# Kernel tuning notes

Hardware: AMD Instinct MI355X
Metric: run time of the kernel (lower is better)

The kernel has to match this reference:

```python
import jax, jax.numpy as jnp
import numpy as np

E, H, L, B = 2048, 32, 1024, 4
S = E // H  # 64
DM, DD = 32, 64


def _ln(x, w, b, eps=1e-5):
    m = x.mean(-1, keepdims=True)
    v = ((x - m) ** 2).mean(-1, keepdims=True)
    return (x - m) / jnp.sqrt(v + eps) * w + b


def setup_inputs() -> dict:
    key = jax.random.key(0)
    ks = jax.random.split(key, 24)
    sc = 0.02  # weight scale for stability
    d = {
        'x': jax.random.normal(ks[0], (B, L, E), jnp.float32),
        'state': jax.random.normal(ks[1], (B, 2 + S, E), jnp.float32) * 0.1,
        'ln1_w': jnp.ones((E,), jnp.float32), 'ln1_b': jnp.zeros((E,), jnp.float32),
        'ln2_w': jnp.ones((E,), jnp.float32), 'ln2_b': jnp.zeros((E,), jnp.float32),
        'maa_x': jax.random.normal(ks[2], (E,), jnp.float32) * 0.1,
        'maa_w1': jax.random.normal(ks[3], (E, 5 * DM), jnp.float32) * sc,
        'maa_w2': jax.random.normal(ks[4], (5, DM, E), jnp.float32) * sc,
        'maa_stack': jax.random.normal(ks[5], (1, 5, E), jnp.float32) * 0.1,
        'time_decay': jax.random.normal(ks[6], (E,), jnp.float32) * 0.5,
        'td_w1': jax.random.normal(ks[7], (E, DD), jnp.float32) * sc,
        'td_w2': jax.random.normal(ks[8], (DD, E), jnp.float32) * sc,
        'u': jax.random.normal(ks[9], (H, S, 1), jnp.float32) * 0.1,
        'Wr': jax.random.normal(ks[10], (E, E), jnp.float32) * sc,
        'Wk': jax.random.normal(ks[11], (E, E), jnp.float32) * sc,
        'Wv': jax.random.normal(ks[12], (E, E), jnp.float32) * sc,
        'Wg': jax.random.normal(ks[13], (E, E), jnp.float32) * sc,
        'Wo': jax.random.normal(ks[14], (E, E), jnp.float32) * sc,
        'gn_w': jnp.ones((E,), jnp.float32), 'gn_b': jnp.zeros((E,), jnp.float32),
        'ffn_maa_k': jax.random.normal(ks[15], (E,), jnp.float32) * 0.1,
        'ffn_maa_r': jax.random.normal(ks[16], (E,), jnp.float32) * 0.1,
        'Wfk': jax.random.normal(ks[17], (E, E), jnp.float32) * sc,
        'Wfr': jax.random.normal(ks[18], (E, E), jnp.float32) * sc,
        'Wfv': jax.random.normal(ks[19], (E, E), jnp.float32) * sc,
    }
    return d


def _block(x, state, ln1_w, ln1_b, ln2_w, ln2_b, maa_x, maa_w1, maa_w2, maa_stack,
           time_decay, td_w1, td_w2, u, Wr, Wk, Wv, Wg, Wo, gn_w, gn_b,
           ffn_maa_k, ffn_maa_r, Wfk, Wfr, Wfv):
    b, l, e = x.shape
    h = u.shape[0]
    s_ = e // h
    # ---- time mixing (parallel over L, sequential WKV scan) ----
    xa = _ln(x, ln1_w, ln1_b)
    # token shift: sx[t] = x[t-1] - x[t], seeded from state row 1
    sx = jnp.concatenate([state[:, 1:2] - xa[:, :1], xa[:, :-1] - xa[:, 1:]], axis=1)
    xxx = jnp.tanh((xa + sx * maa_x) @ maa_w1).reshape(b, l, 5, DM)
    xxx = jnp.einsum('blfd,fde->blfe', xxx, maa_w2)            # [B,L,5,E]
    xm = xa[:, :, None] + sx[:, :, None] * (maa_stack + xxx)   # [B,L,5,E]
    xk, xw, xv, xr, xg = (xm[:, :, j] for j in range(5))       # stack order: k,w,v,r,g
    w = jnp.exp(-jnp.exp(time_decay + jnp.tanh(xw @ td_w1) @ td_w2)).reshape(b, l, h, s_)
    r = (xr @ Wr.T).reshape(b, l, h, s_)
    k = (xk @ Wk.T).reshape(b, l, h, s_)
    v = (xv @ Wv.T).reshape(b, l, h, s_)
    g = jax.nn.silu(xg @ Wg.T)                                 # [B,L,E]
    s0 = state[:, 2:2 + s_].reshape(b, h, s_, s_)              # per-head WKV state

    def step(s, rkvw):
        r_t, k_t, v_t, w_t = rkvw                              # each [B,H,S]
        a = k_t[..., :, None] * v_t[..., None, :]              # outer product [B,H,S,S]
        out = jnp.einsum('bhi,bhij->bhj', r_t, u * a + s)      # [B,H,S]
        s = a + w_t[..., :, None] * s
        return s, out

    rkvw = tuple(jnp.moveaxis(t, 1, 0) for t in (r, k, v, w))  # [L,B,H,S]
    _, out = jax.lax.scan(step, s0, rkvw)
    out = jnp.moveaxis(out, 0, 1).reshape(b, l, e)             # [B,L,E]
    # group norm over heads (eps=1e-5)
    og = out.reshape(b, l, h, s_)
    m = og.mean(-1, keepdims=True)
    va = ((og - m) ** 2).mean(-1, keepdims=True)
    og = ((og - m) / jnp.sqrt(va + 1e-5)).reshape(b, l, e) * gn_w + gn_b
    x1 = x + (og * g) @ Wo.T
    # ---- channel mixing ----
    xc = _ln(x1, ln2_w, ln2_b)
    sx2 = jnp.concatenate([state[:, 0:1] - xc[:, :1], xc[:, :-1] - xc[:, 1:]], axis=1)
    xk2 = xc + sx2 * ffn_maa_k
    xr2 = xc + sx2 * ffn_maa_r
    rr = jax.nn.sigmoid(xr2 @ Wfr.T)
    kk = jnp.square(jax.nn.relu(xk2 @ Wfk.T))
    return x1 + rr * (kk @ Wfv.T)


def reference(x, state, ln1_w, ln1_b, ln2_w, ln2_b, maa_x, maa_w1, maa_w2, maa_stack,
              time_decay, td_w1, td_w2, u, Wr, Wk, Wv, Wg, Wo, gn_w, gn_b,
              ffn_maa_k, ffn_maa_r, Wfk, Wfr, Wfv):
    return _block(x, state, ln1_w, ln1_b, ln2_w, ln2_b, maa_x, maa_w1, maa_w2, maa_stack,
                  time_decay, td_w1, td_w2, u, Wr, Wk, Wv, Wg, Wo, gn_w, gn_b,
                  ffn_maa_k, ffn_maa_r, Wfk, Wfr, Wfv)
```

## Files before the change

### kernel.cpp

```cpp
#include <hip/hip_runtime.h>


#define E     2048
#define LL    1024
#define HHH   32
#define SSS   64
#define NBL   4096
#define NBLE  8388608

typedef short bf16x8 __attribute__((ext_vector_type(8)));
typedef float f32x4  __attribute__((ext_vector_type(4)));
using u16 = unsigned short;

__device__ __forceinline__ u16 f2b(float f) {
    union { float f; unsigned int u; } c; c.f = f;
    unsigned int u = c.u;
    unsigned int r = (u + 0x7fffu + ((u >> 16) & 1u)) >> 16;
    return (u16)r;
}
__device__ __forceinline__ float b2f(u16 b) {
    union { unsigned int u; float f; } c; c.u = ((unsigned int)b) << 16; return c.f;
}

__device__ __forceinline__ float wave_sum(float v) {
#pragma unroll
    for (int m = 32; m >= 1; m >>= 1) v += __shfl_xor(v, m, 64);
    return v;
}

__device__ __forceinline__ void gl_lds16(const void* g, void* l) {
    __builtin_amdgcn_global_load_lds((const __attribute__((address_space(1))) unsigned int*)g,
                                     (__attribute__((address_space(3))) unsigned int*)l, 16, 0, 0);
}


__global__ __launch_bounds__(256) void k_convert(const float* __restrict__ in,
                                                 u16* __restrict__ out, int n) {
    int i = (blockIdx.x * 256 + threadIdx.x) * 4;
    if (i >= n) return;
    float4 v = *reinterpret_cast<const float4*>(in + i);
    ushort4 o = make_ushort4(f2b(v.x), f2b(v.y), f2b(v.z), f2b(v.w));
    *reinterpret_cast<ushort4*>(out + i) = o;
}

__global__ __launch_bounds__(256) void k_transpose(const float* __restrict__ in,
                                                   u16* __restrict__ out, int R, int C) {
    int i = blockIdx.x * 256 + threadIdx.x;
    if (i >= R * C) return;
    int r = i / C, c = i - r * C;
    out[c * R + r] = f2b(in[i]);
}

__global__ __launch_bounds__(256) void k_ln(const float* __restrict__ x,
                                            const float* __restrict__ w,
                                            const float* __restrict__ b,
                                            float* __restrict__ out) {
    int row = blockIdx.x, tid = threadIdx.x;
    const float* xr = x + (size_t)row * E + tid * 8;
    float4 v0 = *reinterpret_cast<const float4*>(xr);
    float4 v1 = *reinterpret_cast<const float4*>(xr + 4);
    float s = v0.x + v0.y + v0.z + v0.w + v1.x + v1.y + v1.z + v1.w;
    __shared__ float red[4];
    s = wave_sum(s);
    int wid = tid >> 6, lane = tid & 63;
    if (lane == 0) red[wid] = s;
    __syncthreads();
    float mean = (red[0] + red[1] + red[2] + red[3]) * (1.0f / E);
    __syncthreads();
    float q = 0.f;
    q += (v0.x - mean) * (v0.x - mean); q += (v0.y - mean) * (v0.y - mean);
    q += (v0.z - mean) * (v0.z - mean); q += (v0.w - mean) * (v0.w - mean);
    q += (v1.x - mean) * (v1.x - mean); q += (v1.y - mean) * (v1.y - mean);
    q += (v1.z - mean) * (v1.z - mean); q += (v1.w - mean) * (v1.w - mean);
    q = wave_sum(q);
    if (lane == 0) red[wid] = q;
    __syncthreads();
    float inv = rsqrtf((red[0] + red[1] + red[2] + red[3]) * (1.0f / E) + 1e-5f);
    int e = tid * 8;
    float4 w0 = *reinterpret_cast<const float4*>(w + e);
    float4 w1 = *reinterpret_cast<const float4*>(w + e + 4);
    float4 b0 = *reinterpret_cast<const float4*>(b + e);
    float4 b1 = *reinterpret_cast<const float4*>(b + e + 4);
    float4 o0, o1;
    o0.x = (v0.x - mean) * inv * w0.x + b0.x; o0.y = (v0.y - mean) * inv * w0.y + b0.y;
    o0.z = (v0.z - mean) * inv * w0.z + b0.z; o0.w = (v0.w - mean) * inv * w0.w + b0.w;
    o1.x = (v1.x - mean) * inv * w1.x + b1.x; o1.y = (v1.y - mean) * inv * w1.y + b1.y;
    o1.z = (v1.z - mean) * inv * w1.z + b1.z; o1.w = (v1.w - mean) * inv * w1.w + b1.w;
    float* op = out + (size_t)row * E + e;
    *reinterpret_cast<float4*>(op) = o0;
    *reinterpret_cast<float4*>(op + 4) = o1;
}

__global__ __launch_bounds__(256) void k_mk(const float* __restrict__ xa,
                                            const float* __restrict__ state,
                                            const float* __restrict__ maa_x,
                                            u16* __restrict__ out) {
    int i = (blockIdx.x * 256 + threadIdx.x) * 4;
    if (i >= NBLE) return;
    int n = i >> 11, e = i & (E - 1);
    int l = n & (LL - 1), b = n >> 10;
    float4 cur = *reinterpret_cast<const float4*>(xa + i);
    float4 prev;
    if (l > 0) prev = *reinterpret_cast<const float4*>(xa + i - E);
    else       prev = *reinterpret_cast<const float4*>(state + (size_t)b * 66 * E + E + e);
    float4 m = *reinterpret_cast<const float4*>(maa_x + e);
    ushort4 o = make_ushort4(f2b(cur.x + (prev.x - cur.x) * m.x),
                             f2b(cur.y + (prev.y - cur.y) * m.y),
                             f2b(cur.z + (prev.z - cur.z) * m.z),
                             f2b(cur.w + (prev.w - cur.w) * m.w));
    *reinterpret_cast<ushort4*>(out + i) = o;
}

__global__ __launch_bounds__(256) void k_mix2(const float* __restrict__ xc,
                                              const float* __restrict__ state,
                                              const float* __restrict__ mk,
                                              const float* __restrict__ mr,
                                              u16* __restrict__ xk2,
                                              u16* __restrict__ xr2) {
    int i = (blockIdx.x * 256 + threadIdx.x) * 4;
    if (i >= NBLE) return;
    int n = i >> 11, e = i & (E - 1);
    int l = n & (LL - 1), b = n >> 10;
    float4 cur = *reinterpret_cast<const float4*>(xc + i);
    float4 prev;
    if (l > 0) prev = *reinterpret_cast<const float4*>(xc + i - E);
    else       prev = *reinterpret_cast<const float4*>(state + (size_t)b * 66 * E + e);
    float4 sx = make_float4(prev.x - cur.x, prev.y - cur.y, prev.z - cur.z, prev.w - cur.w);
    float4 k4 = *reinterpret_cast<const float4*>(mk + e);
    float4 r4 = *reinterpret_cast<const float4*>(mr + e);
    ushort4 ok = make_ushort4(f2b(cur.x + sx.x * k4.x), f2b(cur.y + sx.y * k4.y),
                              f2b(cur.z + sx.z * k4.z), f2b(cur.w + sx.w * k4.w));
    ushort4 orr = make_ushort4(f2b(cur.x + sx.x * r4.x), f2b(cur.y + sx.y * r4.y),
                               f2b(cur.z + sx.z * r4.z), f2b(cur.w + sx.w * r4.w));
    *reinterpret_cast<ushort4*>(xk2 + i) = ok;
    *reinterpret_cast<ushort4*>(xr2 + i) = orr;
}

__global__ __launch_bounds__(256) void k_gnorm(const float* __restrict__ wkv,
                                               const u16* __restrict__ g,
                                               const float* __restrict__ gw,
                                               const float* __restrict__ gb,
                                               u16* __restrict__ ogg) {
    int gidx = blockIdx.x * 4 + (threadIdx.x >> 6);
    int lane = threadIdx.x & 63;
    int n = gidx >> 5, h = gidx & 31;
    size_t base = (size_t)n * E + h * SSS;
    float v = wkv[base + lane];
    float mean = wave_sum(v) * (1.0f / SSS);
    float d = v - mean;
    float var = wave_sum(d * d) * (1.0f / SSS);
    float norm = d * rsqrtf(var + 1e-5f);
    int e = h * SSS + lane;
    float res = norm * gw[e] + gb[e];
    float gv = b2f(g[base + lane]);
    ogg[base + lane] = f2b(res * gv);
}

#define CT 16

__global__ __launch_bounds__(512) void k_scan(const u16* __restrict__ Rb,
                                              const u16* __restrict__ Kb,
                                              const u16* __restrict__ Vb,
                                              const float* __restrict__ W,
                                              const float* __restrict__ state,
                                              const float* __restrict__ u,
                                              float* __restrict__ out) {
    __shared__ u16   ldsR[2][CT * 64];
    __shared__ u16   ldsK[2][CT * 64];
    __shared__ float ldsW[2][CT * 64];
    __shared__ u16   ldsV[2][CT * 32];
    const int blk = blockIdx.x;
    const int b = blk >> 6;
    const int rem = blk & 63;
    const int h = rem >> 1, jh = rem & 1;
    const int tid = threadIdx.x;
    const int wvid = tid >> 6;
    const int lane = tid & 63;
    const int ig = lane >> 2;
    const int jl = lane & 3;
    const int jv = wvid * 4 + jl;
    const int j  = jh * 32 + jv;
    const int i0 = ig * 4;
    float s[4], uu[4];
    const float* s0 = state + (size_t)b * 66 * E + 2 * E + h * (SSS * SSS);
#pragma unroll
    for (int ii = 0; ii < 4; ii++) {
        s[ii] = s0[(i0 + ii) * SSS + j];
        uu[ii] = u[h * SSS + i0 + ii];
    }
    const size_t off0 = (size_t)b * LL * E + h * SSS;

    auto stage = [&](int c, int bufsel) {
        size_t base = off0 + (size_t)c * CT * E;
        if (wvid == 0) {
            const u16* g0 = Rb + base + (size_t)(lane >> 3) * E + ((lane & 7) << 3);
            gl_lds16(g0,         &ldsR[bufsel][lane * 8]);
            gl_lds16(g0 + 8 * E, &ldsR[bufsel][512 + lane * 8]);
        } else if (wvid == 1) {
            const u16* g0 = Kb + base + (size_t)(lane >> 3) * E + ((lane & 7) << 3);
            gl_lds16(g0,         &ldsK[bufsel][lane * 8]);
            gl_lds16(g0 + 8 * E, &ldsK[bufsel][512 + lane * 8]);
        } else if (wvid == 2) {
            const float* g0 = W + base + (size_t)(lane >> 4) * E + ((lane & 15) << 2);
            gl_lds16(g0,         &ldsW[bufsel][lane * 4]);
            gl_lds16(g0 + 4 * E, &ldsW[bufsel][256 + lane * 4]);
        } else if (wvid == 3) {
            const float* g0 = W + base + (size_t)(8 + (lane >> 4)) * E + ((lane & 15) << 2);
            gl_lds16(g0,         &ldsW[bufsel][512 + lane * 4]);
            gl_lds16(g0 + 4 * E, &ldsW[bufsel][768 + lane * 4]);
        } else if (wvid == 4) {
            const u16* g0 = Vb + base + (size_t)(lane >> 2) * E + jh * 32 + ((lane & 3) << 3);
            gl_lds16(g0, &ldsV[bufsel][lane * 8]);
        }
    };

    stage(0, 0);
    __syncthreads();
    int cur = 0;
    for (int c = 0; c < LL / CT; c++) {
        if (c + 1 < LL / CT) stage(c + 1, cur ^ 1);
        size_t offt = off0 + (size_t)c * CT * E + j;
#pragma unroll
        for (int tt = 0; tt < CT; tt++) {
            ushort4 rv = *reinterpret_cast<const ushort4*>(&ldsR[cur][tt * 64 + i0]);
            ushort4 kv = *reinterpret_cast<const ushort4*>(&ldsK[cur][tt * 64 + i0]);
            float4  wv = *reinterpret_cast<const float4*>(&ldsW[cur][tt * 64 + i0]);
            float vj = b2f(ldsV[cur][tt * 32 + jv]);
            float acc = 0.f, a;
            a = b2f(kv.x) * vj; acc += b2f(rv.x) * fmaf(uu[0], a, s[0]); s[0] = fmaf(wv.x, s[0], a);
            a = b2f(kv.y) * vj; acc += b2f(rv.y) * fmaf(uu[1], a, s[1]); s[1] = fmaf(wv.y, s[1], a);
            a = b2f(kv.z) * vj; acc += b2f(rv.z) * fmaf(uu[2], a, s[2]); s[2] = fmaf(wv.z, s[2], a);
            a = b2f(kv.w) * vj; acc += b2f(rv.w) * fmaf(uu[3], a, s[3]); s[3] = fmaf(wv.w, s[3], a);
            acc += __shfl_xor(acc, 4, 64);
            acc += __shfl_xor(acc, 8, 64);
            acc += __shfl_xor(acc, 16, 64);
            acc += __shfl_xor(acc, 32, 64);
            if (ig == 0) out[offt + (size_t)tt * E] = acc;
        }
        __syncthreads();
        cur ^= 1;
    }
}

template <int EP>
__global__ __launch_bounds__(256) void k_gemm128(const u16* __restrict__ A, int lda,
                                                 const u16* __restrict__ Bw,
                                                 void* __restrict__ C, int K,
                                                 const float* __restrict__ evec,
                                                 const float* __restrict__ emat1,
                                                 const float* __restrict__ emat2) {
    __shared__ u16 As[128 * 32];
    __shared__ u16 Bs[128 * 32];
    const int tid = threadIdx.x;
    const int m0 = blockIdx.y << 7, n0 = blockIdx.x << 7;
    const int srow = tid >> 2;
    const int scol = (((tid & 3) ^ ((srow >> 1) & 3)) << 3);
    const int wv = tid >> 6, lane = tid & 63;
    const int wy = (wv >> 1) << 6, wx = (wv & 1) << 6;
    const int lr = lane & 15, lq = lane >> 4;
    const int cofs = ((lq ^ ((lr >> 1) & 3)) << 3);
    f32x4 acc[4][4];
#pragma unroll
    for (int a = 0; a < 4; a++)
#pragma unroll
        for (int bq = 0; bq < 4; bq++) acc[a][bq] = {0.f, 0.f, 0.f, 0.f};
    const u16* gA = A + (size_t)(m0 + srow) * lda + scol;
    const u16* gB = Bw + (size_t)(n0 + srow) * K + scol;
    u16* lA = As + srow * 32 + ((tid & 3) << 3);
    u16* lB = Bs + srow * 32 + ((tid & 3) << 3);
    for (int k0 = 0; k0 < K; k0 += 32) {
        gl_lds16(gA + k0, lA);
        gl_lds16(gA + (size_t)64 * lda + k0, lA + 64 * 32);
        gl_lds16(gB + k0, lB);
        gl_lds16(gB + (size_t)64 * K + k0, lB + 64 * 32);
        __syncthreads();
        bf16x8 af[4], bfr[4];
#pragma unroll
        for (int mt = 0; mt < 4; mt++)
            af[mt] = *reinterpret_cast<const bf16x8*>(As + (wy + mt * 16 + lr) * 32 + cofs);
#pragma unroll
        for (int nt = 0; nt < 4; nt++)
            bfr[nt] = *reinterpret_cast<const bf16x8*>(Bs + (wx + nt * 16 + lr) * 32 + cofs);
#pragma unroll
        for (int mt = 0; mt < 4; mt++)
#pragma unroll
            for (int nt = 0; nt < 4; nt++)
                acc[mt][nt] = __builtin_amdgcn_mfma_f32_16x16x32_bf16(af[mt], bfr[nt], acc[mt][nt], 0, 0, 0);
        __syncthreads();
    }
    const int gmb = m0 + wy + (lq << 2);
    const int gnb = n0 + wx + lr;
#pragma unroll
    for (int mt = 0; mt < 4; mt++) {
#pragma unroll
        for (int nt = 0; nt < 4; nt++) {
            int gn = gnb + nt * 16;
#pragma unroll
            for (int i = 0; i < 4; i++) {
                int gm = gmb + mt * 16 + i;
                size_t idx = (size_t)gm * E + gn;
                float v = acc[mt][nt][i];
                if constexpr (EP == 2) {
                    int l = gm & (LL - 1), bb = gm >> 10;
                    float cur = emat1[idx];
                    float prev = (l > 0) ? emat1[idx - E]
                                         : emat2[(size_t)bb * 66 * E + E + gn];
                    ((u16*)C)[idx] = f2b(cur + (prev - cur) * (evec[gn] + v));
                }
                else if constexpr (EP == 3) ((float*)C)[idx] = expf(-expf(evec[gn] + v));
                else if constexpr (EP == 5) ((float*)C)[idx] = emat1[idx] + v;
                else if constexpr (EP == 6) ((float*)C)[idx] = 1.f / (1.f + expf(-v));
                else if constexpr (EP == 7) { float t = fmaxf(v, 0.f); ((u16*)C)[idx] = f2b(t * t); }
                else if constexpr (EP == 8) ((float*)C)[idx] = emat1[idx] + emat2[idx] * v;
                else if constexpr (EP == 9) ((u16*)C)[idx] = f2b(v);
                else if constexpr (EP == 10) { float sg = 1.f / (1.f + expf(-v)); ((u16*)C)[idx] = f2b(v * sg); }
            }
        }
    }
}

#define BK  32
#define LDP 40

template <int EP>
__global__ __launch_bounds__(256) void k_gemm(const u16* __restrict__ A, int lda,
                                              const u16* __restrict__ Bw,
                                              void* __restrict__ C,
                                              int M, int N, int K) {
    __shared__ u16 As[64 * LDP];
    __shared__ u16 Bs[64 * LDP];
    const int tid = threadIdx.x;
    const int m0 = blockIdx.y << 6, n0 = blockIdx.x << 6;
    const int srow = tid >> 2, skc = (tid & 3) << 3;
    const int lane = tid & 63, wv = tid >> 6;
    const int wr = (wv >> 1) << 5, wc = (wv & 1) << 5;
    const int lr = lane & 15, lq = lane >> 4;
    f32x4 acc[2][2];
#pragma unroll
    for (int a = 0; a < 2; a++)
#pragma unroll
        for (int bq = 0; bq < 2; bq++) acc[a][bq] = {0.f, 0.f, 0.f, 0.f};
    const u16* aptr = A + (size_t)(m0 + srow) * lda + skc;
    const u16* bptr = Bw + (size_t)(n0 + srow) * K + skc;
    const bool bvalid = (n0 + srow) < N;
    for (int k0 = 0; k0 < K; k0 += BK) {
        float4 av = *reinterpret_cast<const float4*>(aptr + k0);
        float4 bv = bvalid ? *reinterpret_cast<const float4*>(bptr + k0)
                           : make_float4(0.f, 0.f, 0.f, 0.f);
        __syncthreads();
        *reinterpret_cast<float4*>(As + srow * LDP + skc) = av;
        *reinterpret_cast<float4*>(Bs + srow * LDP + skc) = bv;
        __syncthreads();
        bf16x8 a0 = *reinterpret_cast<const bf16x8*>(As + (wr + lr) * LDP + lq * 8);
        bf16x8 a1 = *reinterpret_cast<const bf16x8*>(As + (wr + 16 + lr) * LDP + lq * 8);
        bf16x8 b0 = *reinterpret_cast<const bf16x8*>(Bs + (wc + lr) * LDP + lq * 8);
        bf16x8 b1 = *reinterpret_cast<const bf16x8*>(Bs + (wc + 16 + lr) * LDP + lq * 8);
        acc[0][0] = __builtin_amdgcn_mfma_f32_16x16x32_bf16(a0, b0, acc[0][0], 0, 0, 0);
        acc[0][1] = __builtin_amdgcn_mfma_f32_16x16x32_bf16(a0, b1, acc[0][1], 0, 0, 0);
        acc[1][0] = __builtin_amdgcn_mfma_f32_16x16x32_bf16(a1, b0, acc[1][0], 0, 0, 0);
        acc[1][1] = __builtin_amdgcn_mfma_f32_16x16x32_bf16(a1, b1, acc[1][1], 0, 0, 0);
    }
    const int gmb = m0 + wr + lq * 4;
    const int gnb = n0 + wc + lr;
#pragma unroll
    for (int mi = 0; mi < 2; mi++) {
#pragma unroll
        for (int ni = 0; ni < 2; ni++) {
            int gn = gnb + ni * 16;
            if (gn >= N) continue;
#pragma unroll
            for (int i = 0; i < 4; i++) {
                int gm = gmb + mi * 16 + i;
                size_t idx = (size_t)gm * N + gn;
                float v = acc[mi][ni][i];
                if constexpr (EP == 1) ((u16*)C)[idx] = f2b(tanhf(v));
            }
        }
    }
}


extern "C" void kernel_launch(void* const* d_in, const int* in_sizes, int n_in,
                              void* d_out, int out_size, void* d_ws, size_t ws_size,
                              hipStream_t stream) {
    const float* x          = (const float*)d_in[0];
    const float* state      = (const float*)d_in[1];
    const float* ln1_w      = (const float*)d_in[2];
    const float* ln1_b      = (const float*)d_in[3];
    const float* ln2_w      = (const float*)d_in[4];
    const float* ln2_b      = (const float*)d_in[5];
    const float* maa_x      = (const float*)d_in[6];
    const float* maa_w1     = (const float*)d_in[7];
    const float* maa_w2     = (const float*)d_in[8];
    const float* maa_stack  = (const float*)d_in[9];
    const float* time_decay = (const float*)d_in[10];
    const float* td_w1      = (const float*)d_in[11];
    const float* td_w2      = (const float*)d_in[12];
    const float* u          = (const float*)d_in[13];
    const float* Wr         = (const float*)d_in[14];
    const float* Wk         = (const float*)d_in[15];
    const float* Wv         = (const float*)d_in[16];
    const float* Wg         = (const float*)d_in[17];
    const float* Wo         = (const float*)d_in[18];
    const float* gn_w       = (const float*)d_in[19];
    const float* gn_b       = (const float*)d_in[20];
    const float* ffn_k      = (const float*)d_in[21];
    const float* ffn_r      = (const float*)d_in[22];
    const float* Wfk        = (const float*)d_in[23];
    const float* Wfr        = (const float*)d_in[24];
    const float* Wfv        = (const float*)d_in[25];

    char* ws = (char*)d_ws;
    float* R0 = (float*)(ws);
    float* R1 = (float*)(ws + 33554432);
    u16*   R2 = (u16*)(ws + 67108864);
    u16*   R3 = (u16*)(ws + 83886080);
    u16*   R4 = (u16*)(ws + 100663296);
    u16*   R5 = (u16*)(ws + 117440512);
    u16*   R6 = (u16*)(ws + 134217728);
    u16*   WB = (u16*)(ws + 150994944);
    u16*   Hx = (u16*)(ws + 159383552);
    u16*   Ht = (u16*)(ws + 160694272);
    u16*  WT1 = (u16*)(ws + 161218560);
    u16*  WT2 = (u16*)(ws + 161873920);
    u16*  WT3 = (u16*)(ws + 162529280);
    u16*  WT4 = (u16*)(ws + 162791424);

    dim3 blk(256);
    dim3 g128(16, 32);
    dim3 g160(3, 64), g64(1, 64);
    const int ncv = (E * E / 4) / 256;
    const int nel = NBLE / 1024;

    k_transpose<<<(E * 160 + 255) / 256, blk, 0, stream>>>(maa_w1, WT1, E, 160);
    for (int f = 0; f < 5; f++)
        k_transpose<<<(32 * E + 255) / 256, blk, 0, stream>>>(maa_w2 + f * 32 * E, WT2 + f * E * 32, 32, E);
    k_transpose<<<(E * 64 + 255) / 256, blk, 0, stream>>>(td_w1, WT3, E, 64);
    k_transpose<<<(64 * E + 255) / 256, blk, 0, stream>>>(td_w2, WT4, 64, E);

    k_ln<<<NBL, blk, 0, stream>>>(x, ln1_w, ln1_b, R0);
    k_mk<<<nel, blk, 0, stream>>>(R0, state, maa_x, R2);
    k_gemm<1><<<g160, blk, 0, stream>>>(R2, E, WT1, Hx, NBL, 160, E);

    k_gemm128<2><<<g128, blk, 0, stream>>>(Hx + 1 * 32, 160, WT2 + 1 * E * 32, R2, 32,
                                           maa_stack + 1 * E, R0, state);
    k_gemm<1><<<g64, blk, 0, stream>>>(R2, E, WT3, Ht, NBL, 64, E);
    k_gemm128<3><<<g128, blk, 0, stream>>>(Ht, 64, WT4, R1, 64, time_decay, nullptr, nullptr);

    k_gemm128<2><<<g128, blk, 0, stream>>>(Hx + 0 * 32, 160, WT2 + 0 * E * 32, R2, 32,
                                           maa_stack + 0 * E, R0, state);
    k_convert<<<ncv, blk, 0, stream>>>(Wk, WB, E * E);
    k_gemm128<9><<<g128, blk, 0, stream>>>(R2, E, WB, R4, E, nullptr, nullptr, nullptr);

    k_gemm128<2><<<g128, blk, 0, stream>>>(Hx + 2 * 32, 160, WT2 + 2 * E * 32, R2, 32,
                                           maa_stack + 2 * E, R0, state);
    k_convert<<<ncv, blk, 0, stream>>>(Wv, WB, E * E);
    k_gemm128<9><<<g128, blk, 0, stream>>>(R2, E, WB, R5, E, nullptr, nullptr, nullptr);

    k_gemm128<2><<<g128, blk, 0, stream>>>(Hx + 4 * 32, 160, WT2 + 4 * E * 32, R2, 32,
                                           maa_stack + 4 * E, R0, state);
    k_convert<<<ncv, blk, 0, stream>>>(Wg, WB, E * E);
    k_gemm128<10><<<g128, blk, 0, stream>>>(R2, E, WB, R6, E, nullptr, nullptr, nullptr);

    k_gemm128<2><<<g128, blk, 0, stream>>>(Hx + 3 * 32, 160, WT2 + 3 * E * 32, R2, 32,
                                           maa_stack + 3 * E, R0, state);
    k_convert<<<ncv, blk, 0, stream>>>(Wr, WB, E * E);
    k_gemm128<9><<<g128, blk, 0, stream>>>(R2, E, WB, R3, E, nullptr, nullptr, nullptr);

    k_scan<<<256, dim3(512), 0, stream>>>(R3, R4, R5, R1, state, u, R0);
    k_gnorm<<<NBL * HHH / 4, blk, 0, stream>>>(R0, R6, gn_w, gn_b, R6);

    k_convert<<<ncv, blk, 0, stream>>>(Wo, WB, E * E);
    k_gemm128<5><<<g128, blk, 0, stream>>>(R6, E, WB, R0, E, nullptr, x, nullptr);

    k_ln<<<NBL, blk, 0, stream>>>(R0, ln2_w, ln2_b, R1);
    k_mix2<<<nel, blk, 0, stream>>>(R1, state, ffn_k, ffn_r, R2, R3);
    k_convert<<<ncv, blk, 0, stream>>>(Wfk, WB, E * E);
    k_gemm128<7><<<g128, blk, 0, stream>>>(R2, E, WB, R4, E, nullptr, nullptr, nullptr);
    k_convert<<<ncv, blk, 0, stream>>>(Wfr, WB, E * E);
    k_gemm128<6><<<g128, blk, 0, stream>>>(R3, E, WB, R1, E, nullptr, nullptr, nullptr);
    k_convert<<<ncv, blk, 0, stream>>>(Wfv, WB, E * E);
    k_gemm128<8><<<g128, blk, 0, stream>>>(R4, E, WB, (float*)d_out, E, nullptr, R0, R1);
}
```

Baseline: 1.158 ms.

## Split WKV scan into more, smaller blocks and batch shuffle reductions per chunk

```diff
diff --git a/kernel.cpp b/kernel.cpp
--- a/kernel.cpp
+++ b/kernel.cpp
@@ -158,7 +158,7 @@
 
 #define CT 16
 
-__global__ __launch_bounds__(512) void k_scan(const u16* __restrict__ Rb,
+__global__ __launch_bounds__(256) void k_scan(const u16* __restrict__ Rb,
                                               const u16* __restrict__ Kb,
                                               const u16* __restrict__ Vb,
                                               const float* __restrict__ W,
@@ -168,18 +168,18 @@
     __shared__ u16   ldsR[2][CT * 64];
     __shared__ u16   ldsK[2][CT * 64];
     __shared__ float ldsW[2][CT * 64];
-    __shared__ u16   ldsV[2][CT * 32];
+    __shared__ u16   ldsV[2][CT * 16];
     const int blk = blockIdx.x;
-    const int b = blk >> 6;
-    const int rem = blk & 63;
-    const int h = rem >> 1, jh = rem & 1;
+    const int bh = blk & 127;
+    const int jq = blk >> 7;
+    const int b = bh >> 5, h = bh & 31;
     const int tid = threadIdx.x;
     const int wvid = tid >> 6;
     const int lane = tid & 63;
     const int ig = lane >> 2;
     const int jl = lane & 3;
     const int jv = wvid * 4 + jl;
-    const int j  = jh * 32 + jv;
+    const int j  = jq * 16 + jv;
     const int i0 = ig * 4;
     float s[4], uu[4];
     const float* s0 = state + (size_t)b * 66 * E + 2 * E + h * (SSS * SSS);
@@ -196,6 +196,10 @@
             const u16* g0 = Rb + base + (size_t)(lane >> 3) * E + ((lane & 7) << 3);
             gl_lds16(g0,         &ldsR[bufsel][lane * 8]);
             gl_lds16(g0 + 8 * E, &ldsR[bufsel][512 + lane * 8]);
+            if (lane < 32) {
+                const u16* gv = Vb + base + (size_t)(lane >> 1) * E + jq * 16 + ((lane & 1) << 3);
+                gl_lds16(gv, &ldsV[bufsel][lane * 8]);
+            }
         } else if (wvid == 1) {
             const u16* g0 = Kb + base + (size_t)(lane >> 3) * E + ((lane & 7) << 3);
             gl_lds16(g0,         &ldsK[bufsel][lane * 8]);
@@ -204,13 +208,10 @@
             const float* g0 = W + base + (size_t)(lane >> 4) * E + ((lane & 15) << 2);
             gl_lds16(g0,         &ldsW[bufsel][lane * 4]);
             gl_lds16(g0 + 4 * E, &ldsW[bufsel][256 + lane * 4]);
-        } else if (wvid == 3) {
+        } else {
             const float* g0 = W + base + (size_t)(8 + (lane >> 4)) * E + ((lane & 15) << 2);
             gl_lds16(g0,         &ldsW[bufsel][512 + lane * 4]);
             gl_lds16(g0 + 4 * E, &ldsW[bufsel][768 + lane * 4]);
-        } else if (wvid == 4) {
-            const u16* g0 = Vb + base + (size_t)(lane >> 2) * E + jh * 32 + ((lane & 3) << 3);
-            gl_lds16(g0, &ldsV[bufsel][lane * 8]);
         }
     };
 
@@ -219,23 +220,32 @@
     int cur = 0;
     for (int c = 0; c < LL / CT; c++) {
         if (c + 1 < LL / CT) stage(c + 1, cur ^ 1);
-        size_t offt = off0 + (size_t)c * CT * E + j;
+        float accs[CT];
 #pragma unroll
         for (int tt = 0; tt < CT; tt++) {
             ushort4 rv = *reinterpret_cast<const ushort4*>(&ldsR[cur][tt * 64 + i0]);
             ushort4 kv = *reinterpret_cast<const ushort4*>(&ldsK[cur][tt * 64 + i0]);
             float4  wv = *reinterpret_cast<const float4*>(&ldsW[cur][tt * 64 + i0]);
-            float vj = b2f(ldsV[cur][tt * 32 + jv]);
+            float vj = b2f(ldsV[cur][tt * 16 + jv]);
             float acc = 0.f, a;
             a = b2f(kv.x) * vj; acc += b2f(rv.x) * fmaf(uu[0], a, s[0]); s[0] = fmaf(wv.x, s[0], a);
             a = b2f(kv.y) * vj; acc += b2f(rv.y) * fmaf(uu[1], a, s[1]); s[1] = fmaf(wv.y, s[1], a);
             a = b2f(kv.z) * vj; acc += b2f(rv.z) * fmaf(uu[2], a, s[2]); s[2] = fmaf(wv.z, s[2], a);
             a = b2f(kv.w) * vj; acc += b2f(rv.w) * fmaf(uu[3], a, s[3]); s[3] = fmaf(wv.w, s[3], a);
-            acc += __shfl_xor(acc, 4, 64);
-            acc += __shfl_xor(acc, 8, 64);
-            acc += __shfl_xor(acc, 16, 64);
-            acc += __shfl_xor(acc, 32, 64);
-            if (ig == 0) out[offt + (size_t)tt * E] = acc;
+            accs[tt] = acc;
+        }
+#pragma unroll
+        for (int tt = 0; tt < CT; tt++) accs[tt] += __shfl_xor(accs[tt], 4, 64);
+#pragma unroll
+        for (int tt = 0; tt < CT; tt++) accs[tt] += __shfl_xor(accs[tt], 8, 64);
+#pragma unroll
+        for (int tt = 0; tt < CT; tt++) accs[tt] += __shfl_xor(accs[tt], 16, 64);
+#pragma unroll
+        for (int tt = 0; tt < CT; tt++) accs[tt] += __shfl_xor(accs[tt], 32, 64);
+        if (ig == 0) {
+            size_t offt = off0 + (size_t)c * CT * E + j;
+#pragma unroll
+            for (int tt = 0; tt < CT; tt++) out[offt + (size_t)tt * E] = accs[tt];
         }
         __syncthreads();
         cur ^= 1;
@@ -467,7 +477,7 @@
     k_convert<<<ncv, blk, 0, stream>>>(Wr, WB, E * E);
     k_gemm128<9><<<g128, blk, 0, stream>>>(R2, E, WB, R3, E, nullptr, nullptr, nullptr);
 
-    k_scan<<<256, dim3(512), 0, stream>>>(R3, R4, R5, R1, state, u, R0);
+    k_scan<<<512, blk, 0, stream>>>(R3, R4, R5, R1, state, u, R0);
     k_gnorm<<<NBL * HHH / 4, blk, 0, stream>>>(R0, R6, gn_w, gn_b, R6);
 
     k_convert<<<ncv, blk, 0, stream>>>(Wo, WB, E * E);
```

Measured after the change: 1.102 ms. -4.8%, faster.
